# Kernel tuning notes

Measured on AMD Instinct MI355X. Metric: run time of the kernel, lower is better.

The kernel has to match this reference:

```python
import jax, jax.numpy as jnp
import numpy as np

B, C_IN, H, W = 4, 128, 32, 128   # W must equal out_channels (fc_out acts on last dim)
C_OUT, NUM_HEADS = 128, 2
BN_EPS = 1e-5


def setup_inputs() -> dict:
    key = jax.random.key(0)
    ks = jax.random.split(key, 14)
    s = 0.05  # small init scale for weights
    d = {
        "x": jax.random.normal(ks[0], (B, C_IN, H, W), jnp.float32),
        "wq": jax.random.normal(ks[1], (C_OUT, C_IN), jnp.float32) * s,
        "bq": jax.random.normal(ks[2], (C_OUT,), jnp.float32) * s,
        "wk": jax.random.normal(ks[3], (C_OUT, C_IN), jnp.float32) * s,
        "bk": jax.random.normal(ks[4], (C_OUT,), jnp.float32) * s,
        "wv": jax.random.normal(ks[5], (C_OUT, C_IN), jnp.float32) * s,
        "bv": jax.random.normal(ks[6], (C_OUT,), jnp.float32) * s,
        "fc_w": jax.random.normal(ks[7], (C_OUT, C_OUT), jnp.float32) * s,
        "fc_b": jax.random.normal(ks[8], (C_OUT,), jnp.float32) * s,
        "bn_gamma": jnp.ones((C_OUT,), jnp.float32),
        "bn_beta": jnp.zeros((C_OUT,), jnp.float32),
        "bn_mean": jax.random.normal(ks[9], (C_OUT,), jnp.float32) * 0.1,
        "bn_var": jax.random.uniform(ks[10], (C_OUT,), jnp.float32, 0.5, 1.5),
        "prelu_a": jnp.full((1,), 0.25, jnp.float32),
    }
    return d


def reference(x, wq, bq, wk, bk, wv, bv, fc_w, fc_b,
              bn_gamma, bn_beta, bn_mean, bn_var, prelu_a):
    b, c_in, h, w = x.shape
    c_out = wq.shape[0]
    nh = NUM_HEADS
    dk = c_out // nh
    L = h * w
    xf = x.reshape(b, c_in, L)                                # (B, Cin, L)
    # 1x1 convs == per-token linear projections
    q = jnp.einsum('oi,bil->bol', wq, xf) + bq[:, None]       # (B, Cout, L)
    k = jnp.einsum('oi,bil->bol', wk, xf) + bk[:, None]
    v = jnp.einsum('oi,bil->bol', wv, xf) + bv[:, None]
    Q = q.reshape(b, nh, dk, L)                               # (B, h, d_k, L)
    K = k.reshape(b, nh, dk, L)
    V = v.reshape(b, nh, dk, L)
    # scaled dot-product attention over the L = H*W tokens
    scores = jnp.einsum('bhdl,bhdm->bhlm', Q, K) / jnp.sqrt(jnp.float32(dk))
    attn = jax.nn.softmax(scores, axis=-1)                    # (B, h, L, L)
    out = jnp.einsum('bhlm,bhdm->bhdl', attn, V)              # (B, h, d_k, L)
    out = out.reshape(b, c_out, h, w)                         # (B, Cout, H, W)
    # fc_out: torch Linear on the LAST dim (W == Cout)
    y = jnp.einsum('bchw,ow->bcho', out, fc_w) + fc_b         # (B, Cout, H, W)
    # BatchNorm2d (eval mode: running stats) over channel dim
    inv = jax.lax.rsqrt(bn_var + BN_EPS)
    y = (y - bn_mean[None, :, None, None]) * (inv * bn_gamma)[None, :, None, None] \
        + bn_beta[None, :, None, None]
    # PReLU (single shared slope); dropout is identity in eval
    y = jnp.where(y > 0, y, prelu_a[0] * y)
    return y
```

## Files before the change

kernel.cpp:

```cpp
#include <hip/hip_runtime.h>

typedef _Float16 f16x8 __attribute__((ext_vector_type(8)));
typedef _Float16 f16x4t __attribute__((ext_vector_type(4)));
typedef __fp16 h16x2 __attribute__((ext_vector_type(2)));
typedef float f32x4 __attribute__((ext_vector_type(4)));
typedef float f32x16 __attribute__((ext_vector_type(16)));
typedef unsigned int uint2v __attribute__((ext_vector_type(2)));

#define L_SZ 4096

__device__ __forceinline__ unsigned short f2h(float f) {
    _Float16 h = (_Float16)f;
    return __builtin_bit_cast(unsigned short, h);
}
__device__ __forceinline__ unsigned int pk2(float a, float b) {
    h16x2 p = __builtin_amdgcn_cvt_pkrtz(a, b);
    return __builtin_bit_cast(unsigned int, p);
}
__device__ __forceinline__ float fexp2(float x) {
#if __has_builtin(__builtin_amdgcn_exp2f)
    return __builtin_amdgcn_exp2f(x);
#else
    return exp2f(x);
#endif
}
__device__ __forceinline__ float frcp(float x) {
#if __has_builtin(__builtin_amdgcn_rcpf)
    return __builtin_amdgcn_rcpf(x);
#else
    return 1.0f / x;
#endif
}
__device__ __forceinline__ void async16(unsigned short* lds, const unsigned short* g) {
    __builtin_amdgcn_global_load_lds(
        (const __attribute__((address_space(1))) unsigned int*)g,
        (__attribute__((address_space(3))) unsigned int*)lds, 16, 0, 0);
}

#define SLOT(row, ci) ((((ci) * 64) + ((row) & 32) + (((row) & 31) ^ (ci))) * 8)

__global__ __launch_bounds__(256) void prep_kernel(
    const float* __restrict__ wq, const float* __restrict__ wk,
    const float* __restrict__ wv, const float* __restrict__ fcw,
    unsigned short* __restrict__ Wimg, unsigned short* __restrict__ Fimg)
{
    int e2 = blockIdx.x * 256 + threadIdx.x;
    if (e2 < 24576) {
        const float* src = (e2 < 8192) ? wq : (e2 < 16384 ? wk : wv);
        float2 v = *(const float2*)&src[(e2 * 2) & 16383];
        int e = e2 * 2;
        int o = e >> 7, ci = (e & 127) >> 3, j = e & 7;
        *(unsigned int*)&Wimg[o * 128 + ((ci ^ (o & 15)) * 8) + j] = pk2(v.x, v.y);
    } else {
        int fe = (e2 - 24576) * 2;
        float2 v = *(const float2*)&fcw[fe];
        int o = fe >> 7, ci = (fe & 127) >> 3, j = fe & 7;
        *(unsigned int*)&Fimg[o * 128 + ((ci ^ (o & 15)) * 8) + j] = pk2(v.x, v.y);
    }
}

__global__ __launch_bounds__(256, 3) void qkv_kernel(
    const float* __restrict__ x,
    const unsigned short* __restrict__ Wimg,
    const float* __restrict__ bq, const float* __restrict__ bk,
    const float* __restrict__ bv,
    unsigned short* __restrict__ Qp, unsigned short* __restrict__ Kp,
    unsigned short* __restrict__ Vp)
{
    int raw = blockIdx.x;
    int v = (raw & 7) * 96 + (raw >> 3);
    int tile = v / 3;
    int p = v - tile * 3;
    int bidx = tile >> 6;
    int l0 = (tile & 63) * 64;
    int tid = threadIdx.x;
    int wave = tid >> 6, lane = tid & 63;
    int c = lane & 15, qd = lane >> 4;

    __shared__ __align__(16) unsigned short Ws[128 * 128];
    __shared__ __align__(16) unsigned short Sc[9216];

    const unsigned short* wsrc = Wimg + p * 16384;
    #pragma unroll
    for (int t = 0; t < 8; ++t)
        async16(&Ws[(t * 256 + wave * 64) * 8], &wsrc[(size_t)(t * 256 + wave * 64 + lane) * 8]);

    unsigned short* Xs = Sc;
    #pragma unroll
    for (int it = 0; it < 8; ++it) {
        int i  = (tid >> 4) + 16 * it;
        int l4 = (tid & 15) * 4;
        const float4 vx = *(const float4*)&x[(bidx * 128 + i) * L_SZ + l0 + l4];
        float vv[4] = {vx.x, vx.y, vx.z, vx.w};
        int ci = i >> 3;
        #pragma unroll
        for (int u = 0; u < 4; ++u) {
            int l = l4 + u;
            Xs[l * 128 + ((ci ^ (l & 15)) * 8) + (i & 7)] = f2h(vv[u]);
        }
    }
    __syncthreads();

    f16x8 afrag[4];
    #pragma unroll
    for (int kc = 0; kc < 4; ++kc) {
        int l = wave * 16 + c;
        int ci = kc * 4 + qd;
        afrag[kc] = *(const f16x8*)&Xs[l * 128 + ((ci ^ (l & 15)) * 8)];
    }
    __syncthreads();

    f32x4 acc[8];
    #pragma unroll
    for (int nt = 0; nt < 8; ++nt) acc[nt] = (f32x4){0.f, 0.f, 0.f, 0.f};

    #pragma unroll
    for (int kc = 0; kc < 4; ++kc) {
        #pragma unroll
        for (int nt = 0; nt < 8; ++nt) {
            int o = nt * 16 + c;
            f16x8 bfrag = *(const f16x8*)&Ws[o * 128 + (((kc * 4 + qd) ^ c) * 8)];
            acc[nt] = __builtin_amdgcn_mfma_f32_16x16x32_f16(afrag[kc], bfrag, acc[nt], 0, 0, 0);
        }
    }

    const float s_q = 0.18033688011f;
    if (p < 2) {
        const float* bias = (p == 0) ? bq : bk;
        unsigned short* Ot = Sc;
        #pragma unroll
        for (int nt = 0; nt < 8; ++nt) {
            int o = nt * 16 + c;
            float bo = bias[o];
            #pragma unroll
            for (int r = 0; r < 4; ++r) {
                int ll = wave * 16 + qd * 4 + r;
                float val = acc[nt][r] + bo;
                if (p == 0) val *= s_q;
                Ot[ll * 144 + o] = f2h(val);
            }
        }
        __syncthreads();
        unsigned short* dst = (p == 0) ? Qp : Kp;
        #pragma unroll
        for (int t = 0; t < 4; ++t) {
            int u = tid + t * 256;
            int row = u >> 4, col = (u & 15) * 8;
            int h = col >> 6, d = col & 63;
            uint4 a = *(const uint4*)&Ot[row * 144 + col];
            *(uint4*)&dst[((size_t)(bidx * 2 + h) * L_SZ + l0 + row) * 64 + d] = a;
        }
    } else {
        unsigned short* Vt = Sc;
        #pragma unroll
        for (int nt = 0; nt < 8; ++nt) {
            int o = nt * 16 + c;
            #pragma unroll
            for (int r = 0; r < 4; ++r) {
                int ll = wave * 16 + qd * 4 + r;
                Vt[o * 72 + ll] = f2h(acc[nt][r] + bv[o]);
            }
        }
        __syncthreads();
        #pragma unroll
        for (int t = 0; t < 2; ++t) {
            int u = tid + t * 256;
            int row = u >> 2;
            int lc = (u & 3) * 16;
            uint4 a0 = *(const uint4*)&Vt[row * 72 + lc];
            uint4 a1 = *(const uint4*)&Vt[row * 72 + lc + 8];
            *(uint4*)&Vp[(size_t)(bidx * 128 + row) * L_SZ + l0 + lc] = a0;
            *(uint4*)&Vp[(size_t)(bidx * 128 + row) * L_SZ + l0 + lc + 8] = a1;
        }
    }
}

__global__ __launch_bounds__(256, 4) void attn_kernel(
    const unsigned short* __restrict__ Qp, const unsigned short* __restrict__ Kp,
    const unsigned short* __restrict__ Vp,
    unsigned short* __restrict__ Opart, float* __restrict__ Mpart, float* __restrict__ Lpart)
{
    int raw = blockIdx.x;
    int blk = (raw & 7) * 128 + (raw >> 3);
    int lt = blk & 31;
    int bh = (blk >> 5) & 7;
    int sp = blk >> 8;
    int l0 = lt * 128;
    int tid = threadIdx.x;
    int wave = tid >> 6, lane = tid & 63;
    int ln = lane & 31, hi = lane >> 5;
    int b = bh >> 1, h = bh & 1;

    __shared__ __align__(16) unsigned short Ks[2][4096];
    __shared__ __align__(16) unsigned short Vs[2][4096];

    const unsigned short* Qb = Qp + (size_t)bh * L_SZ * 64;
    const unsigned short* Kb = Kp + (size_t)bh * L_SZ * 64;
    const unsigned short* Vb = Vp + ((size_t)b * 128 + h * 64) * L_SZ;

    int lq = l0 + wave * 32 + ln;
    f16x8 qf[4];
    #pragma unroll
    for (int kc = 0; kc < 4; ++kc)
        qf[kc] = *(const f16x8*)&Qb[(size_t)lq * 64 + kc * 16 + hi * 8];

    float m_st = -1e30f, lsum = 0.f;
    f32x16 acc0 = {}, acc1 = {};

    int mglob = sp * 1024;
    int ci0 = wave, ci1 = 4 + wave;
    int r0_ = (lane & 32) | ((lane & 31) ^ ci0);
    int r1_ = (lane & 32) | ((lane & 31) ^ ci1);

#define STAGE(t, buf) do {                                                        \
        int m0_ = mglob + (t) * 64;                                               \
        async16(&Ks[buf][(wave * 64) * 8],       &Kb[(size_t)(m0_ + r0_) * 64 + ci0 * 8]); \
        async16(&Ks[buf][(256 + wave * 64) * 8], &Kb[(size_t)(m0_ + r1_) * 64 + ci1 * 8]); \
        async16(&Vs[buf][(wave * 64) * 8],       &Vb[(size_t)r0_ * L_SZ + m0_ + ci0 * 8]); \
        async16(&Vs[buf][(256 + wave * 64) * 8], &Vb[(size_t)r1_ * L_SZ + m0_ + ci1 * 8]); \
    } while (0)

    STAGE(0, 0);

    for (int it = 0; it < 16; ++it) {
        int cur = it & 1;
        __syncthreads();
        if (it < 15) STAGE(it + 1, cur ^ 1);

        __builtin_amdgcn_s_setprio(1);
        f32x16 s0 = {}, s1 = {};
        #pragma unroll
        for (int kc = 0; kc < 4; ++kc) {
            int cd = kc * 2 + hi;
            f16x8 k0 = *(const f16x8*)&Ks[cur][SLOT(ln, cd)];
            f16x8 k1 = *(const f16x8*)&Ks[cur][SLOT(32 + ln, cd)];
            s0 = __builtin_amdgcn_mfma_f32_32x32x16_f16(k0, qf[kc], s0, 0, 0, 0);
            s1 = __builtin_amdgcn_mfma_f32_32x32x16_f16(k1, qf[kc], s1, 0, 0, 0);
        }

        float t[8];
        #pragma unroll
        for (int r = 0; r < 8; ++r)
            t[r] = fmaxf(fmaxf(s0[r], s0[r + 8]), s1[r]);
        #pragma unroll
        for (int r = 0; r < 4; ++r)
            t[r] = fmaxf(fmaxf(t[r], t[r + 4]), s1[8 + r]);
        float m01 = fmaxf(fmaxf(t[0], t[1]), s1[12]);
        float m23 = fmaxf(fmaxf(t[2], t[3]), s1[13]);
        float mx = fmaxf(fmaxf(m01, m23), fmaxf(s1[14], s1[15]));
        mx = fmaxf(mx, __shfl_xor(mx, 32));

        if (!__all(mx <= m_st + 8.0f)) {
            float mnew = fmaxf(m_st, mx);
            float alpha = fexp2(m_st - mnew);
            m_st = mnew;
            lsum *= alpha;
            #pragma unroll
            for (int r = 0; r < 16; ++r) { acc0[r] *= alpha; acc1[r] *= alpha; }
        }
        float rs0 = 0.f, rs1 = 0.f, rs2 = 0.f, rs3 = 0.f;
        #pragma unroll
        for (int r = 0; r < 4; ++r) {
            float p0 = fexp2(s0[r]      - m_st); s0[r]      = p0; rs0 += p0;
            float p1 = fexp2(s0[r + 4]  - m_st); s0[r + 4]  = p1; rs1 += p1;
            float p2 = fexp2(s0[r + 8]  - m_st); s0[r + 8]  = p2; rs2 += p2;
            float p3 = fexp2(s0[r + 12] - m_st); s0[r + 12] = p3; rs3 += p3;
        }
        #pragma unroll
        for (int r = 0; r < 4; ++r) {
            float p0 = fexp2(s1[r]      - m_st); s1[r]      = p0; rs0 += p0;
            float p1 = fexp2(s1[r + 4]  - m_st); s1[r + 4]  = p1; rs1 += p1;
            float p2 = fexp2(s1[r + 8]  - m_st); s1[r + 8]  = p2; rs2 += p2;
            float p3 = fexp2(s1[r + 12] - m_st); s1[r + 12] = p3; rs3 += p3;
        }
        lsum += (rs0 + rs1) + (rs2 + rs3);

        #pragma unroll
        for (int kc = 0; kc < 4; ++kc) {
            unsigned int a0, a1, a2, a3;
            if (kc == 0) {
                a0 = pk2(s0[0], s0[1]);  a1 = pk2(s0[2], s0[3]);
                a2 = pk2(s0[4], s0[5]);  a3 = pk2(s0[6], s0[7]);
            } else if (kc == 1) {
                a0 = pk2(s0[8], s0[9]);  a1 = pk2(s0[10], s0[11]);
                a2 = pk2(s0[12], s0[13]); a3 = pk2(s0[14], s0[15]);
            } else if (kc == 2) {
                a0 = pk2(s1[0], s1[1]);  a1 = pk2(s1[2], s1[3]);
                a2 = pk2(s1[4], s1[5]);  a3 = pk2(s1[6], s1[7]);
            } else {
                a0 = pk2(s1[8], s1[9]);  a1 = pk2(s1[10], s1[11]);
                a2 = pk2(s1[12], s1[13]); a3 = pk2(s1[14], s1[15]);
            }
            uint2v r02 = __builtin_amdgcn_permlane32_swap(a0, a2, false, false);
            uint2v r13 = __builtin_amdgcn_permlane32_swap(a1, a3, false, false);
            uint4 pw; pw.x = r02[0]; pw.y = r13[0]; pw.z = r02[1]; pw.w = r13[1];
            f16x8 pf = __builtin_bit_cast(f16x8, pw);
            int cd = kc * 2 + hi;
            f16x8 v0 = *(const f16x8*)&Vs[cur][SLOT(ln, cd)];
            f16x8 v1 = *(const f16x8*)&Vs[cur][SLOT(32 + ln, cd)];
            acc0 = __builtin_amdgcn_mfma_f32_32x32x16_f16(v0, pf, acc0, 0, 0, 0);
            acc1 = __builtin_amdgcn_mfma_f32_32x32x16_f16(v1, pf, acc1, 0, 0, 0);
        }
        __builtin_amdgcn_s_setprio(0);
    }
#undef STAGE

    float l_tot = lsum + __shfl_xor(lsum, 32);
    unsigned short* Ow = Opart + (size_t)(sp * 8 + bh) * 64 * 4096;
    #pragma unroll
    for (int r = 0; r < 16; ++r) {
        int d0 = (r & 3) + 8 * (r >> 2) + 4 * hi;
        Ow[(size_t)d0 * 4096 + lq] = f2h(acc0[r]);
        Ow[(size_t)(32 + d0) * 4096 + lq] = f2h(acc1[r]);
    }
    if (hi == 0) {
        Mpart[(sp * 8 + bh) * 4096 + lq] = m_st;
        Lpart[(sp * 8 + bh) * 4096 + lq] = l_tot;
    }
}

__global__ __launch_bounds__(256) void scl_kernel(
    const float* __restrict__ Mp, const float* __restrict__ Lp,
    unsigned short* __restrict__ SclImg)
{
    int gid = blockIdx.x * 256 + threadIdx.x;
    int bh = gid >> 12, l = gid & 4095;
    float m0 = Mp[(0 * 8 + bh) * 4096 + l], m1 = Mp[(1 * 8 + bh) * 4096 + l];
    float m2 = Mp[(2 * 8 + bh) * 4096 + l], m3 = Mp[(3 * 8 + bh) * 4096 + l];
    float mx = fmaxf(fmaxf(m0, m1), fmaxf(m2, m3));
    float a0 = fexp2(m0 - mx), a1 = fexp2(m1 - mx);
    float a2 = fexp2(m2 - mx), a3 = fexp2(m3 - mx);
    float den = a0 * Lp[(0 * 8 + bh) * 4096 + l] + a1 * Lp[(1 * 8 + bh) * 4096 + l]
              + a2 * Lp[(2 * 8 + bh) * 4096 + l] + a3 * Lp[(3 * 8 + bh) * 4096 + l];
    float inv = frcp(den);
    int hl = l >> 7, ww = l & 127;
    int slot = hl * 128 + ((ww + hl) & 127);
    uint2 sc;
    sc.x = pk2(a0 * inv, a1 * inv);
    sc.y = pk2(a2 * inv, a3 * inv);
    *(uint2*)&SclImg[((size_t)bh * 4096 + slot) * 4] = sc;
}

__global__ __launch_bounds__(256, 2) void fc_kernel(
    const unsigned short* __restrict__ Opart,
    const unsigned short* __restrict__ SclImg,
    const unsigned short* __restrict__ Fimg,
    const float* __restrict__ fc_b, const float* __restrict__ bn_g,
    const float* __restrict__ bn_b, const float* __restrict__ bn_m,
    const float* __restrict__ bn_v, const float* __restrict__ prelu_a,
    float* __restrict__ out)
{
    int raw = blockIdx.x;
    int blk = (raw & 7) * 64 + (raw >> 3);
    int r0 = blk * 32;
    int tid = threadIdx.x;
    int c0 = blk & 127;
    int bh = blk >> 6;
    int d = c0 & 63;

    int wave = tid >> 6, lane = tid & 63;
    int c = lane & 15, qd = lane >> 4;
    int rw = r0 + (wave >> 1) * 16;
    int o0 = (wave & 1) * 64;
    int hh = (rw + c) & 31;

    __shared__ __align__(16) unsigned short Fw[128 * 128];
    __shared__ __align__(16) unsigned short SclU[4096 * 4];

    #pragma unroll
    for (int t = 0; t < 8; ++t)
        async16(&SclU[(t * 256 + wave * 64) * 8],
                &SclImg[(size_t)bh * 16384 + (size_t)(t * 256 + wave * 64 + lane) * 8]);
    #pragma unroll
    for (int t = 0; t < 8; ++t)
        async16(&Fw[(t * 256 + wave * 64) * 8],
                &Fimg[(size_t)(t * 256 + wave * 64 + lane) * 8]);

    uint4 ovr[4][4];
    #pragma unroll
    for (int kc = 0; kc < 4; ++kc) {
        int w0 = kc * 32 + qd * 8;
        #pragma unroll
        for (int s = 0; s < 4; ++s)
            ovr[kc][s] = *(const uint4*)&Opart[(size_t)(s * 8 + bh) * 262144 + (size_t)d * 4096 + hh * 128 + w0];
    }
    __syncthreads();

    f16x8 af[4];
    #pragma unroll
    for (int kc = 0; kc < 4; ++kc) {
        int w0 = kc * 32 + qd * 8;
        f16x8 ov0 = __builtin_bit_cast(f16x8, ovr[kc][0]);
        f16x8 ov1 = __builtin_bit_cast(f16x8, ovr[kc][1]);
        f16x8 ov2 = __builtin_bit_cast(f16x8, ovr[kc][2]);
        f16x8 ov3 = __builtin_bit_cast(f16x8, ovr[kc][3]);
        #pragma unroll
        for (int j = 0; j < 8; ++j) {
            int slot = hh * 128 + ((w0 + j + hh) & 127);
            f16x4t sc = *(const f16x4t*)&SclU[slot * 4];
            float v = (float)ov0[j] * (float)sc[0] + (float)ov1[j] * (float)sc[1]
                    + (float)ov2[j] * (float)sc[2] + (float)ov3[j] * (float)sc[3];
            af[kc][j] = (_Float16)v;
        }
    }

    f32x4 acc[4];
    #pragma unroll
    for (int nt = 0; nt < 4; ++nt) acc[nt] = (f32x4){0.f, 0.f, 0.f, 0.f};
    #pragma unroll
    for (int kc = 0; kc < 4; ++kc) {
        #pragma unroll
        for (int nt = 0; nt < 4; ++nt) {
            int o = o0 + nt * 16 + c;
            f16x8 bf = *(const f16x8*)&Fw[o * 128 + (((kc * 4 + qd) ^ c) * 8)];
            acc[nt] = __builtin_amdgcn_mfma_f32_16x16x32_f16(af[kc], bf, acc[nt], 0, 0, 0);
        }
    }

    float pa = prelu_a[0];
    float g  = bn_g[c0] * rsqrtf(bn_v[c0] + 1e-5f);
    float mn = bn_m[c0], bt = bn_b[c0];
    #pragma unroll
    for (int r = 0; r < 4; ++r) {
        int orow = rw + qd * 4 + r;
        #pragma unroll
        for (int nt = 0; nt < 4; ++nt) {
            int o = o0 + nt * 16 + c;
            float y = (acc[nt][r] + fc_b[o] - mn) * g + bt;
            y = y > 0.f ? y : pa * y;
            out[(size_t)orow * 128 + o] = y;
        }
    }
}

extern "C" void kernel_launch(void* const* d_in, const int* in_sizes, int n_in,
                              void* d_out, int out_size, void* d_ws, size_t ws_size,
                              hipStream_t stream) {
    const float* x     = (const float*)d_in[0];
    const float* wq    = (const float*)d_in[1];
    const float* bq    = (const float*)d_in[2];
    const float* wk    = (const float*)d_in[3];
    const float* bk    = (const float*)d_in[4];
    const float* wv    = (const float*)d_in[5];
    const float* bv    = (const float*)d_in[6];
    const float* fcw_f = (const float*)d_in[7];
    const float* fcb   = (const float*)d_in[8];
    const float* bn_g  = (const float*)d_in[9];
    const float* bn_b  = (const float*)d_in[10];
    const float* bn_m  = (const float*)d_in[11];
    const float* bn_v  = (const float*)d_in[12];
    const float* pa    = (const float*)d_in[13];
    float* out = (float*)d_out;

    unsigned short* Qp  = (unsigned short*)d_ws;
    unsigned short* Kp  = Qp + 8 * L_SZ * 64;
    unsigned short* Vp  = Kp + 8 * L_SZ * 64;
    unsigned short* Opart = Vp + 8 * L_SZ * 64;
    float* Mpart = (float*)(Opart + 4 * 8 * 64 * L_SZ);
    float* Lpart = Mpart + 4 * 8 * L_SZ;
    unsigned short* Wimg   = (unsigned short*)(Lpart + 4 * 8 * L_SZ);
    unsigned short* Fimg   = Wimg + 384 * 128;
    unsigned short* SclImg = Fimg + 128 * 128;

    hipLaunchKernelGGL(prep_kernel, dim3(128),  dim3(256), 0, stream,
                       wq, wk, wv, fcw_f, Wimg, Fimg);
    hipLaunchKernelGGL(qkv_kernel,  dim3(768),  dim3(256), 0, stream,
                       x, Wimg, bq, bk, bv, Qp, Kp, Vp);
    hipLaunchKernelGGL(attn_kernel, dim3(1024), dim3(256), 0, stream,
                       Qp, Kp, Vp, Opart, Mpart, Lpart);
    hipLaunchKernelGGL(scl_kernel,  dim3(128),  dim3(256), 0, stream,
                       Mpart, Lpart, SclImg);
    hipLaunchKernelGGL(fc_kernel,   dim3(512),  dim3(256), 0, stream,
                       Opart, SclImg, Fimg, fcb, bn_g, bn_b, bn_m, bn_v, pa, out);
}
```

Measured before the change: 158.6 us.

## Software-pipeline attention loop to overlap QK^T with previous tile's PV

Restructures the flash-attention main loop so that in each iteration the QK^T MFMAs for tile t are issued alongside the PV MFMAs for tile t-1, followed by the softmax and packing for tile t. The packed probabilities are carried across iterations in registers. V gets a third LDS buffer so it can be prefetched while an older tile is still being read. The aim is to hide the exp/max/pack latency of the softmax behind matrix-core work. The cost is more LDS (a third V buffer) and extra live VGPRs for the carried P fragments. Under the 4-blocks-per-CU launch bound this could cause spills or lower occupancy.

```diff
diff --git a/kernel.cpp b/kernel.cpp
--- a/kernel.cpp
+++ b/kernel.cpp
@@ -192,7 +192,7 @@
     int b = bh >> 1, h = bh & 1;
 
     __shared__ __align__(16) unsigned short Ks[2][4096];
-    __shared__ __align__(16) unsigned short Vs[2][4096];
+    __shared__ __align__(16) unsigned short Vs[3][4096];
 
     const unsigned short* Qb = Qp + (size_t)bh * L_SZ * 64;
     const unsigned short* Kb = Kp + (size_t)bh * L_SZ * 64;
@@ -206,104 +206,137 @@
 
     float m_st = -1e30f, lsum = 0.f;
     f32x16 acc0 = {}, acc1 = {};
+    uint4 pp[4];
 
     int mglob = sp * 1024;
     int ci0 = wave, ci1 = 4 + wave;
     int r0_ = (lane & 32) | ((lane & 31) ^ ci0);
     int r1_ = (lane & 32) | ((lane & 31) ^ ci1);
 
-#define STAGE(t, buf) do {                                                        \
+#define STAGEK(t, kb) do {                                                        \
         int m0_ = mglob + (t) * 64;                                               \
-        async16(&Ks[buf][(wave * 64) * 8],       &Kb[(size_t)(m0_ + r0_) * 64 + ci0 * 8]); \
-        async16(&Ks[buf][(256 + wave * 64) * 8], &Kb[(size_t)(m0_ + r1_) * 64 + ci1 * 8]); \
-        async16(&Vs[buf][(wave * 64) * 8],       &Vb[(size_t)r0_ * L_SZ + m0_ + ci0 * 8]); \
-        async16(&Vs[buf][(256 + wave * 64) * 8], &Vb[(size_t)r1_ * L_SZ + m0_ + ci1 * 8]); \
+        async16(&Ks[kb][(wave * 64) * 8],       &Kb[(size_t)(m0_ + r0_) * 64 + ci0 * 8]); \
+        async16(&Ks[kb][(256 + wave * 64) * 8], &Kb[(size_t)(m0_ + r1_) * 64 + ci1 * 8]); \
     } while (0)
-
-    STAGE(0, 0);
-
-    for (int it = 0; it < 16; ++it) {
-        int cur = it & 1;
+#define STAGEV(t, vb) do {                                                        \
+        int m0_ = mglob + (t) * 64;                                               \
+        async16(&Vs[vb][(wave * 64) * 8],       &Vb[(size_t)r0_ * L_SZ + m0_ + ci0 * 8]); \
+        async16(&Vs[vb][(256 + wave * 64) * 8], &Vb[(size_t)r1_ * L_SZ + m0_ + ci1 * 8]); \
+    } while (0)
+
+#define QK_COMPUTE(kb) do {                                                       \
+        s0 = (f32x16){}; s1 = (f32x16){};                                         \
+        _Pragma("unroll")                                                         \
+        for (int kc = 0; kc < 4; ++kc) {                                          \
+            int cd = kc * 2 + hi;                                                 \
+            f16x8 k0 = *(const f16x8*)&Ks[kb][SLOT(ln, cd)];                      \
+            f16x8 k1 = *(const f16x8*)&Ks[kb][SLOT(32 + ln, cd)];                 \
+            s0 = __builtin_amdgcn_mfma_f32_32x32x16_f16(k0, qf[kc], s0, 0, 0, 0); \
+            s1 = __builtin_amdgcn_mfma_f32_32x32x16_f16(k1, qf[kc], s1, 0, 0, 0); \
+        }                                                                         \
+    } while (0)
+
+#define PV_ACC(vb) do {                                                           \
+        const unsigned short* Vsl = &Vs[vb][0];                                   \
+        _Pragma("unroll")                                                         \
+        for (int kc = 0; kc < 4; ++kc) {                                          \
+            f16x8 pf = __builtin_bit_cast(f16x8, pp[kc]);                         \
+            int cd = kc * 2 + hi;                                                 \
+            f16x8 v0 = *(const f16x8*)&Vsl[SLOT(ln, cd)];                         \
+            f16x8 v1 = *(const f16x8*)&Vsl[SLOT(32 + ln, cd)];                    \
+            acc0 = __builtin_amdgcn_mfma_f32_32x32x16_f16(v0, pf, acc0, 0, 0, 0); \
+            acc1 = __builtin_amdgcn_mfma_f32_32x32x16_f16(v1, pf, acc1, 0, 0, 0); \
+        }                                                                         \
+    } while (0)
+
+#define SOFTMAX_PACK() do {                                                       \
+        float t_[8];                                                              \
+        _Pragma("unroll")                                                         \
+        for (int r = 0; r < 8; ++r)                                               \
+            t_[r] = fmaxf(fmaxf(s0[r], s0[r + 8]), s1[r]);                        \
+        _Pragma("unroll")                                                         \
+        for (int r = 0; r < 4; ++r)                                               \
+            t_[r] = fmaxf(fmaxf(t_[r], t_[r + 4]), s1[8 + r]);                    \
+        float m01 = fmaxf(fmaxf(t_[0], t_[1]), s1[12]);                           \
+        float m23 = fmaxf(fmaxf(t_[2], t_[3]), s1[13]);                           \
+        float mx = fmaxf(fmaxf(m01, m23), fmaxf(s1[14], s1[15]));                 \
+        mx = fmaxf(mx, __shfl_xor(mx, 32));                                       \
+        if (!__all(mx <= m_st + 8.0f)) {                                          \
+            float mnew = fmaxf(m_st, mx);                                         \
+            float alpha = fexp2(m_st - mnew);                                     \
+            m_st = mnew;                                                          \
+            lsum *= alpha;                                                        \
+            _Pragma("unroll")                                                     \
+            for (int r = 0; r < 16; ++r) { acc0[r] *= alpha; acc1[r] *= alpha; }  \
+        }                                                                         \
+        float rs0 = 0.f, rs1 = 0.f, rs2 = 0.f, rs3 = 0.f;                         \
+        _Pragma("unroll")                                                         \
+        for (int r = 0; r < 4; ++r) {                                             \
+            float p0 = fexp2(s0[r]      - m_st); s0[r]      = p0; rs0 += p0;      \
+            float p1 = fexp2(s0[r + 4]  - m_st); s0[r + 4]  = p1; rs1 += p1;      \
+            float p2 = fexp2(s0[r + 8]  - m_st); s0[r + 8]  = p2; rs2 += p2;      \
+            float p3 = fexp2(s0[r + 12] - m_st); s0[r + 12] = p3; rs3 += p3;      \
+        }                                                                         \
+        _Pragma("unroll")                                                         \
+        for (int r = 0; r < 4; ++r) {                                             \
+            float p0 = fexp2(s1[r]      - m_st); s1[r]      = p0; rs0 += p0;      \
+            float p1 = fexp2(s1[r + 4]  - m_st); s1[r + 4]  = p1; rs1 += p1;      \
+            float p2 = fexp2(s1[r + 8]  - m_st); s1[r + 8]  = p2; rs2 += p2;      \
+            float p3 = fexp2(s1[r + 12] - m_st); s1[r + 12] = p3; rs3 += p3;      \
+        }                                                                         \
+        lsum += (rs0 + rs1) + (rs2 + rs3);                                        \
+        _Pragma("unroll")                                                         \
+        for (int kc = 0; kc < 4; ++kc) {                                          \
+            unsigned int a0, a1, a2, a3;                                          \
+            if (kc == 0) {                                                        \
+                a0 = pk2(s0[0], s0[1]);  a1 = pk2(s0[2], s0[3]);                  \
+                a2 = pk2(s0[4], s0[5]);  a3 = pk2(s0[6], s0[7]);                  \
+            } else if (kc == 1) {                                                 \
+                a0 = pk2(s0[8], s0[9]);  a1 = pk2(s0[10], s0[11]);                \
+                a2 = pk2(s0[12], s0[13]); a3 = pk2(s0[14], s0[15]);               \
+            } else if (kc == 2) {                                                 \
+                a0 = pk2(s1[0], s1[1]);  a1 = pk2(s1[2], s1[3]);                  \
+                a2 = pk2(s1[4], s1[5]);  a3 = pk2(s1[6], s1[7]);                  \
+            } else {                                                              \
+                a0 = pk2(s1[8], s1[9]);  a1 = pk2(s1[10], s1[11]);                \
+                a2 = pk2(s1[12], s1[13]); a3 = pk2(s1[14], s1[15]);               \
+            }                                                                     \
+            uint2v r02 = __builtin_amdgcn_permlane32_swap(a0, a2, false, false);  \
+            uint2v r13 = __builtin_amdgcn_permlane32_swap(a1, a3, false, false);  \
+            uint4 pw; pw.x = r02[0]; pw.y = r13[0]; pw.z = r02[1]; pw.w = r13[1]; \
+            pp[kc] = pw;                                                          \
+        }                                                                         \
+    } while (0)
+
+    f32x16 s0, s1;
+
+    STAGEK(0, 0); STAGEV(0, 0);
+    __syncthreads();
+    STAGEK(1, 1); STAGEV(1, 1);
+    __builtin_amdgcn_s_setprio(1);
+    QK_COMPUTE(0);
+    SOFTMAX_PACK();
+    __builtin_amdgcn_s_setprio(0);
+
+    for (int t = 1; t < 16; ++t) {
         __syncthreads();
-        if (it < 15) STAGE(it + 1, cur ^ 1);
+        if (t < 15) { STAGEK(t + 1, (t + 1) & 1); STAGEV(t + 1, (t + 1) % 3); }
 
         __builtin_amdgcn_s_setprio(1);
-        f32x16 s0 = {}, s1 = {};
-        #pragma unroll
-        for (int kc = 0; kc < 4; ++kc) {
-            int cd = kc * 2 + hi;
-            f16x8 k0 = *(const f16x8*)&Ks[cur][SLOT(ln, cd)];
-            f16x8 k1 = *(const f16x8*)&Ks[cur][SLOT(32 + ln, cd)];
-            s0 = __builtin_amdgcn_mfma_f32_32x32x16_f16(k0, qf[kc], s0, 0, 0, 0);
-            s1 = __builtin_amdgcn_mfma_f32_32x32x16_f16(k1, qf[kc], s1, 0, 0, 0);
-        }
-
-        float t[8];
-        #pragma unroll
-        for (int r = 0; r < 8; ++r)
-            t[r] = fmaxf(fmaxf(s0[r], s0[r + 8]), s1[r]);
-        #pragma unroll
-        for (int r = 0; r < 4; ++r)
-            t[r] = fmaxf(fmaxf(t[r], t[r + 4]), s1[8 + r]);
-        float m01 = fmaxf(fmaxf(t[0], t[1]), s1[12]);
-        float m23 = fmaxf(fmaxf(t[2], t[3]), s1[13]);
-        float mx = fmaxf(fmaxf(m01, m23), fmaxf(s1[14], s1[15]));
-        mx = fmaxf(mx, __shfl_xor(mx, 32));
-
-        if (!__all(mx <= m_st + 8.0f)) {
-            float mnew = fmaxf(m_st, mx);
-            float alpha = fexp2(m_st - mnew);
-            m_st = mnew;
-            lsum *= alpha;
-            #pragma unroll
-            for (int r = 0; r < 16; ++r) { acc0[r] *= alpha; acc1[r] *= alpha; }
-        }
-        float rs0 = 0.f, rs1 = 0.f, rs2 = 0.f, rs3 = 0.f;
-        #pragma unroll
-        for (int r = 0; r < 4; ++r) {
-            float p0 = fexp2(s0[r]      - m_st); s0[r]      = p0; rs0 += p0;
-            float p1 = fexp2(s0[r + 4]  - m_st); s0[r + 4]  = p1; rs1 += p1;
-            float p2 = fexp2(s0[r + 8]  - m_st); s0[r + 8]  = p2; rs2 += p2;
-            float p3 = fexp2(s0[r + 12] - m_st); s0[r + 12] = p3; rs3 += p3;
-        }
-        #pragma unroll
-        for (int r = 0; r < 4; ++r) {
-            float p0 = fexp2(s1[r]      - m_st); s1[r]      = p0; rs0 += p0;
-            float p1 = fexp2(s1[r + 4]  - m_st); s1[r + 4]  = p1; rs1 += p1;
-            float p2 = fexp2(s1[r + 8]  - m_st); s1[r + 8]  = p2; rs2 += p2;
-            float p3 = fexp2(s1[r + 12] - m_st); s1[r + 12] = p3; rs3 += p3;
-        }
-        lsum += (rs0 + rs1) + (rs2 + rs3);
-
-        #pragma unroll
-        for (int kc = 0; kc < 4; ++kc) {
-            unsigned int a0, a1, a2, a3;
-            if (kc == 0) {
-                a0 = pk2(s0[0], s0[1]);  a1 = pk2(s0[2], s0[3]);
-                a2 = pk2(s0[4], s0[5]);  a3 = pk2(s0[6], s0[7]);
-            } else if (kc == 1) {
-                a0 = pk2(s0[8], s0[9]);  a1 = pk2(s0[10], s0[11]);
-                a2 = pk2(s0[12], s0[13]); a3 = pk2(s0[14], s0[15]);
-            } else if (kc == 2) {
-                a0 = pk2(s1[0], s1[1]);  a1 = pk2(s1[2], s1[3]);
-                a2 = pk2(s1[4], s1[5]);  a3 = pk2(s1[6], s1[7]);
-            } else {
-                a0 = pk2(s1[8], s1[9]);  a1 = pk2(s1[10], s1[11]);
-                a2 = pk2(s1[12], s1[13]); a3 = pk2(s1[14], s1[15]);
-            }
-            uint2v r02 = __builtin_amdgcn_permlane32_swap(a0, a2, false, false);
-            uint2v r13 = __builtin_amdgcn_permlane32_swap(a1, a3, false, false);
-            uint4 pw; pw.x = r02[0]; pw.y = r13[0]; pw.z = r02[1]; pw.w = r13[1];
-            f16x8 pf = __builtin_bit_cast(f16x8, pw);
-            int cd = kc * 2 + hi;
-            f16x8 v0 = *(const f16x8*)&Vs[cur][SLOT(ln, cd)];
-            f16x8 v1 = *(const f16x8*)&Vs[cur][SLOT(32 + ln, cd)];
-            acc0 = __builtin_amdgcn_mfma_f32_32x32x16_f16(v0, pf, acc0, 0, 0, 0);
-            acc1 = __builtin_amdgcn_mfma_f32_32x32x16_f16(v1, pf, acc1, 0, 0, 0);
-        }
+        QK_COMPUTE(t & 1);
+        PV_ACC((t - 1) % 3);
+        SOFTMAX_PACK();
         __builtin_amdgcn_s_setprio(0);
     }
-#undef STAGE
+    __builtin_amdgcn_s_setprio(1);
+    PV_ACC(0);
+    __builtin_amdgcn_s_setprio(0);
+
+#undef STAGEK
+#undef STAGEV
+#undef QK_COMPUTE
+#undef PV_ACC
+#undef SOFTMAX_PACK
 
     float l_tot = lsum + __shfl_xor(lsum, 32);
     unsigned short* Ow = Opart + (size_t)(sp * 8 + bh) * 64 * 4096;
```

Measured after the change: 167.9 us. 5.9% more time.
